# Optimization experiments

Measured on AMD Instinct MI355X. Metric: run time of the kernel, lower is better.

## Reference

```python
import jax, jax.numpy as jnp
import numpy as np

B, L = 128, 4096
H, RH, D, K = 128, 64, 64, 512  # num_hiddens, residual_hiddens, embedding_dim, num_embeddings
BETA = 0.25  # commitment_cost


def conv1d(x, w, b=None, stride=1, pad=0):
    # x: (N, C, W); w: (O, I, K) torch layout
    y = jax.lax.conv_general_dilated(x, w, (stride,), [(pad, pad)],
                                     dimension_numbers=('NCW', 'OIW', 'NCW'))
    return y if b is None else y + b[None, :, None]


def convT1d(x, w, b=None, stride=2, pad=1):
    # torch ConvTranspose1d weight layout (in, out, k)
    k = w.shape[-1]
    w_t = jnp.flip(w, -1).transpose(1, 0, 2)  # (out, in, k)
    y = jax.lax.conv_general_dilated(x, w_t, (1,), [(k - 1 - pad, k - 1 - pad)],
                                     lhs_dilation=(stride,),
                                     dimension_numbers=('NCW', 'OIW', 'NCW'))
    return y if b is None else y + b[None, :, None]


def res_stack(x, layers):
    for w1, w2 in layers:
        h = conv1d(jax.nn.relu(x), w1, None, 1, 1)
        h = conv1d(jax.nn.relu(h), w2, None, 1, 0)
        x = x + h
    return jax.nn.relu(x)


def _forward(x, enc_w1, enc_b1, enc_w2, enc_b2, enc_w3, enc_b3,
             enc_r1a, enc_r1b, enc_r2a, enc_r2b, pre_vq_w, pre_vq_b, codebook,
             dec_w1, dec_b1, dec_r1a, dec_r1b, dec_r2a, dec_r2b,
             dec_ct1_w, dec_ct1_b, dec_ct2_w, dec_ct2_b):
    # ---- Encoder (compression_factor == 4) ----
    h = x[:, None, :]                                   # (B, 1, L)
    h = jax.nn.relu(conv1d(h, enc_w1, enc_b1, 2, 1))    # (B, H/2, L/2)
    h = jax.nn.relu(conv1d(h, enc_w2, enc_b2, 2, 1))    # (B, H, L/4)
    h = conv1d(h, enc_w3, enc_b3, 1, 1)
    h = res_stack(h, [(enc_r1a, enc_r1b), (enc_r2a, enc_r2b)])
    z = conv1d(h, pre_vq_w, pre_vq_b, 1, 0)             # (B, D, T)

    # ---- Vector quantization ----
    zt = z.transpose(0, 2, 1)                           # (B, T, D)
    flat = zt.reshape(-1, D)                            # (BT, D)
    dists = (jnp.sum(flat * flat, 1, keepdims=True)
             - 2.0 * flat @ codebook.T
             + jnp.sum(codebook * codebook, 1))         # (BT, K)
    idx = jnp.argmin(dists, axis=1)                     # (BT,)
    q = codebook[idx].reshape(zt.shape)                 # (B, T, D)

    e_latent = jnp.mean((jax.lax.stop_gradient(q) - zt) ** 2)
    q_latent = jnp.mean((q - jax.lax.stop_gradient(zt)) ** 2)
    loss = q_latent + BETA * e_latent
    q_st = zt + jax.lax.stop_gradient(q - zt)           # straight-through

    counts = jnp.zeros((K,), flat.dtype).at[idx].add(1.0)
    probs = counts / idx.shape[0]
    perplexity = jnp.exp(-jnp.sum(probs * jnp.log(probs + 1e-10)))

    # ---- Decoder (compression_factor == 4) ----
    hd = q_st.transpose(0, 2, 1)                        # (B, D, T)
    hd = conv1d(hd, dec_w1, dec_b1, 1, 1)               # (B, H, T)
    hd = res_stack(hd, [(dec_r1a, dec_r1b), (dec_r2a, dec_r2b)])
    hd = jax.nn.relu(convT1d(hd, dec_ct1_w, dec_ct1_b)) # (B, H/2, 2T)
    hd = convT1d(hd, dec_ct2_w, dec_ct2_b)              # (B, 1, 4T)
    recon = jnp.squeeze(hd)                             # (B, L)
    return loss, recon, perplexity


def setup_inputs() -> dict:
    key = jax.random.key(0)
    ks = jax.random.split(key, 32)
    n = lambda i, shape, s=0.05: jax.random.normal(ks[i], shape, jnp.float32) * s
    inp = {
        'x': jax.random.normal(ks[0], (B, L), jnp.float32),
        'enc_w1': n(1, (H // 2, 1, 4)), 'enc_b1': jnp.zeros((H // 2,), jnp.float32),
        'enc_w2': n(2, (H, H // 2, 4)), 'enc_b2': jnp.zeros((H,), jnp.float32),
        'enc_w3': n(3, (H, H, 3)), 'enc_b3': jnp.zeros((H,), jnp.float32),
        'enc_r1a': n(4, (RH, H, 3)), 'enc_r1b': n(5, (H, RH, 1)),
        'enc_r2a': n(6, (RH, H, 3)), 'enc_r2b': n(7, (H, RH, 1)),
        'pre_vq_w': n(8, (D, H, 1)), 'pre_vq_b': jnp.zeros((D,), jnp.float32),
        'codebook': jax.random.uniform(ks[9], (K, D), jnp.float32, -1.0 / K, 1.0 / K),
        'dec_w1': n(10, (H, D, 3)), 'dec_b1': jnp.zeros((H,), jnp.float32),
        'dec_r1a': n(11, (RH, H, 3)), 'dec_r1b': n(12, (H, RH, 1)),
        'dec_r2a': n(13, (RH, H, 3)), 'dec_r2b': n(14, (H, RH, 1)),
        'dec_ct1_w': n(15, (H, H // 2, 4)), 'dec_ct1_b': jnp.zeros((H // 2,), jnp.float32),
        'dec_ct2_w': n(16, (H // 2, 1, 4)), 'dec_ct2_b': jnp.zeros((1,), jnp.float32),
    }
    return inp


def reference(x, enc_w1, enc_b1, enc_w2, enc_b2, enc_w3, enc_b3,
              enc_r1a, enc_r1b, enc_r2a, enc_r2b, pre_vq_w, pre_vq_b, codebook,
              dec_w1, dec_b1, dec_r1a, dec_r1b, dec_r2a, dec_r2b,
              dec_ct1_w, dec_ct1_b, dec_ct2_w, dec_ct2_b):
    return _forward(x, enc_w1, enc_b1, enc_w2, enc_b2, enc_w3, enc_b3,
                    enc_r1a, enc_r1b, enc_r2a, enc_r2b, pre_vq_w, pre_vq_b, codebook,
                    dec_w1, dec_b1, dec_r1a, dec_r1b, dec_r2a, dec_r2b,
                    dec_ct1_w, dec_ct1_b, dec_ct2_w, dec_ct2_b)
```

## Files before the change

### kernel.cpp

```cpp
#include <hip/hip_runtime.h>
#include <hip/hip_bf16.h>
#include <math.h>

using bf16 = __hip_bfloat16;
typedef __attribute__((ext_vector_type(4))) float f32x4;
typedef __attribute__((ext_vector_type(8))) short s16x8;

#define MFMA16(a,b,c) __builtin_amdgcn_mfma_f32_16x16x32_bf16((a),(b),(c),0,0,0)


__device__ inline float bf2f(unsigned short u) {
    union { float f; unsigned v; } c; c.v = ((unsigned)u) << 16; return c.f;
}
__device__ inline unsigned short bfbits(float f) {
    union { bf16 h; unsigned short u; } c; c.h = __float2bfloat16(f); return c.u;
}
__device__ inline s16x8 relu8(s16x8 v) {
#pragma unroll
    for (int j = 0; j < 8; ++j)
        v[j] = (short)(((unsigned short)v[j] & 0x8000u) ? 0 : (unsigned short)v[j]);
    return v;
}

enum { M_S1 = 0, M_S2 = 1, M_CT = 2 };

template<int CIN, int COUT, int NTAP, int MODE, bool RELU_IN, bool RELU_OUT,
         bool HAS_BIAS>
__global__ __launch_bounds__(256) void gconv_k(
    const bf16* __restrict__ in, const bf16* __restrict__ wt,
    const float* __restrict__ bias, bf16* __restrict__ out,
    int Lin, int Lout)
{
    constexpr int T  = (MODE == M_S2) ? 132 : ((MODE == M_CT) ? 66 : (NTAP == 3 ? 66 : 64));
    constexpr int NG = (MODE == M_CT) ? 2 : 1;
    constexpr int WL = (COUT == 128) ? 4 : 2;
    constexpr int KS = CIN / 32;
    constexpr int SOFF = (MODE == M_CT || NTAP == 3) ? -1 : 0;
    __shared__ bf16 sX[T * CIN];

    const int tid = threadIdx.x;
    const int b   = blockIdx.y;
    const int l0  = blockIdx.x * 64;
    const bf16* inb = in + (size_t)b * Lin * CIN;

    constexpr int CPR = CIN / 8;
    for (int i = tid; i < T * CPR; i += 256) {
        int t  = i / CPR;
        int c0 = (i - t * CPR) * 8;
        int g;
        if (MODE == M_S2) g = (t < 66) ? 2 * (l0 + t) : 2 * (l0 + t - 66) - 1;
        else              g = l0 + t + SOFF;
        s16x8 v = {};
        if (g >= 0 && g < Lin) v = *(const s16x8*)(inb + (size_t)g * CIN + c0);
        if (RELU_IN) v = relu8(v);
        int byte = ((t * CIN + c0) << 1) ^ ((t & 7) << 4);
        *(s16x8*)((char*)sX + byte) = v;
    }
    __syncthreads();

    const int lane = tid & 63;
    const int wid  = __builtin_amdgcn_readfirstlane(tid >> 6);
    const int co0  = (COUT == 128) ? wid * 32 : (wid & 1) * 32;
    const int lw0  = (COUT == 128) ? 0 : (wid >> 1) * 32;
    const int lr   = lane & 15;
    const int kg   = lane >> 4;

    f32x4 acc[NG][2][WL];
#pragma unroll
    for (int g = 0; g < NG; ++g)
#pragma unroll
        for (int cf = 0; cf < 2; ++cf)
#pragma unroll
            for (int lf = 0; lf < WL; ++lf)
                acc[g][cf][lf] = (f32x4){0.f, 0.f, 0.f, 0.f};

#pragma unroll
    for (int g = 0; g < NG; ++g) {
#pragma unroll
        for (int k = 0; k < NTAP; ++k) {
            int roff;
            if (MODE == M_S1)      roff = k;
            else if (MODE == M_S2) roff = (k == 0) ? 66 : (k == 1) ? 0 : (k == 2) ? 67 : 1;
            else                   roff = g + k;
            const bf16* Ab = wt + (size_t)(g * NTAP + k) * COUT * CIN;
#pragma unroll
            for (int ks = 0; ks < KS; ++ks) {
                s16x8 af[2];
#pragma unroll
                for (int cf = 0; cf < 2; ++cf)
                    af[cf] = *(const s16x8*)(Ab + (co0 + cf * 16 + lr) * CIN + ks * 32 + kg * 8);
                s16x8 bfr[WL];
#pragma unroll
                for (int lf = 0; lf < WL; ++lf) {
                    int t = roff + lw0 + lf * 16 + lr;
                    int byte = ((t * CIN + ks * 32 + kg * 8) << 1) ^ ((t & 7) << 4);
                    bfr[lf] = *(const s16x8*)((const char*)sX + byte);
                }
#pragma unroll
                for (int cf = 0; cf < 2; ++cf)
#pragma unroll
                    for (int lf = 0; lf < WL; ++lf)
                        acc[g][cf][lf] = MFMA16(af[cf], bfr[lf], acc[g][cf][lf]);
            }
        }
    }

#pragma unroll
    for (int g = 0; g < NG; ++g)
#pragma unroll
        for (int cf = 0; cf < 2; ++cf)
#pragma unroll
            for (int lf = 0; lf < WL; ++lf) {
                int cb0  = co0 + cf * 16 + kg * 4;
                int lcol = lw0 + lf * 16 + lr;
                int gcol = (MODE == M_CT) ? (2 * (l0 + lcol) + g) : (l0 + lcol);
                float r[4];
#pragma unroll
                for (int j = 0; j < 4; ++j) {
                    r[j] = acc[g][cf][lf][j];
                    if (HAS_BIAS) r[j] += bias[cb0 + j];
                    if (RELU_OUT) r[j] = fmaxf(r[j], 0.f);
                }
                bf16* po = out + ((size_t)b * Lout + gcol) * COUT + cb0;
                uint2 pk;
                pk.x = (unsigned)bfbits(r[0]) | ((unsigned)bfbits(r[1]) << 16);
                pk.y = (unsigned)bfbits(r[2]) | ((unsigned)bfbits(r[3]) << 16);
                *(uint2*)po = pk;
            }
}

template<bool RELU_OUT>
__global__ __launch_bounds__(256) void fres_k(
    const bf16* __restrict__ in, const bf16* __restrict__ w1t,
    const bf16* __restrict__ w2t, bf16* __restrict__ out)
{
    __shared__ bf16 sX[66 * 128];
    __shared__ bf16 sH[64 * 64];
    const int tid = threadIdx.x;
    const int b   = blockIdx.y;
    const int l0  = blockIdx.x * 64;
    const bf16* inb = in + (size_t)b * 1024 * 128;

    for (int i = tid; i < 66 * 16; i += 256) {
        int t = i >> 4, c0 = (i & 15) * 8;
        int g = l0 + t - 1;
        s16x8 v = {};
        if (g >= 0 && g < 1024) v = *(const s16x8*)(inb + (size_t)g * 128 + c0);
        int byte = ((t * 128 + c0) << 1) ^ ((t & 7) << 4);
        *(s16x8*)((char*)sX + byte) = v;
    }
    __syncthreads();

    const int lane = tid & 63;
    const int wid  = __builtin_amdgcn_readfirstlane(tid >> 6);
    const int lr   = lane & 15;
    const int kg   = lane >> 4;

    {
        const int co0 = (wid & 1) * 32;
        const int lw0 = (wid >> 1) * 32;
        f32x4 acc[2][2];
#pragma unroll
        for (int cf = 0; cf < 2; ++cf)
#pragma unroll
            for (int lf = 0; lf < 2; ++lf) acc[cf][lf] = (f32x4){0.f, 0.f, 0.f, 0.f};
#pragma unroll
        for (int k = 0; k < 3; ++k) {
            const bf16* Ab = w1t + (size_t)k * 64 * 128;
#pragma unroll
            for (int ks = 0; ks < 4; ++ks) {
                s16x8 af[2];
#pragma unroll
                for (int cf = 0; cf < 2; ++cf)
                    af[cf] = *(const s16x8*)(Ab + (co0 + cf * 16 + lr) * 128 + ks * 32 + kg * 8);
                s16x8 bfr[2];
#pragma unroll
                for (int lf = 0; lf < 2; ++lf) {
                    int t = k + lw0 + lf * 16 + lr;
                    int byte = ((t * 128 + ks * 32 + kg * 8) << 1) ^ ((t & 7) << 4);
                    bfr[lf] = relu8(*(const s16x8*)((const char*)sX + byte));
                }
#pragma unroll
                for (int cf = 0; cf < 2; ++cf)
#pragma unroll
                    for (int lf = 0; lf < 2; ++lf)
                        acc[cf][lf] = MFMA16(af[cf], bfr[lf], acc[cf][lf]);
            }
        }
#pragma unroll
        for (int cf = 0; cf < 2; ++cf)
#pragma unroll
            for (int lf = 0; lf < 2; ++lf) {
                int pos = lw0 + lf * 16 + lr;
                int ch  = co0 + cf * 16 + kg * 4;
                uint2 pk;
                pk.x = (unsigned)bfbits(fmaxf(acc[cf][lf][0], 0.f)) |
                       ((unsigned)bfbits(fmaxf(acc[cf][lf][1], 0.f)) << 16);
                pk.y = (unsigned)bfbits(fmaxf(acc[cf][lf][2], 0.f)) |
                       ((unsigned)bfbits(fmaxf(acc[cf][lf][3], 0.f)) << 16);
                int byte = ((pos * 64 + ch) << 1) ^ ((pos & 7) << 4);
                *(uint2*)((char*)sH + byte) = pk;
            }
    }
    __syncthreads();

    {
        const int co0 = wid * 32;
        f32x4 acc2[2][4];
#pragma unroll
        for (int cf = 0; cf < 2; ++cf)
#pragma unroll
            for (int lf = 0; lf < 4; ++lf) acc2[cf][lf] = (f32x4){0.f, 0.f, 0.f, 0.f};
#pragma unroll
        for (int ks = 0; ks < 2; ++ks) {
            s16x8 af[2];
#pragma unroll
            for (int cf = 0; cf < 2; ++cf)
                af[cf] = *(const s16x8*)(w2t + (size_t)(co0 + cf * 16 + lr) * 64 + ks * 32 + kg * 8);
            s16x8 bfr[4];
#pragma unroll
            for (int lf = 0; lf < 4; ++lf) {
                int t = lf * 16 + lr;
                int byte = ((t * 64 + ks * 32 + kg * 8) << 1) ^ ((t & 7) << 4);
                bfr[lf] = *(const s16x8*)((const char*)sH + byte);
            }
#pragma unroll
            for (int cf = 0; cf < 2; ++cf)
#pragma unroll
                for (int lf = 0; lf < 4; ++lf)
                    acc2[cf][lf] = MFMA16(af[cf], bfr[lf], acc2[cf][lf]);
        }
#pragma unroll
        for (int cf = 0; cf < 2; ++cf)
#pragma unroll
            for (int lf = 0; lf < 4; ++lf) {
                int cb0  = co0 + cf * 16 + kg * 4;
                int lcol = lf * 16 + lr;
                int tX   = lcol + 1;
                int rbyte = ((tX * 128 + cb0) << 1) ^ ((tX & 7) << 4);
                uint2 old = *(const uint2*)((const char*)sX + rbyte);
                float r[4];
                r[0] = acc2[cf][lf][0] + bf2f((unsigned short)(old.x & 0xffff));
                r[1] = acc2[cf][lf][1] + bf2f((unsigned short)(old.x >> 16));
                r[2] = acc2[cf][lf][2] + bf2f((unsigned short)(old.y & 0xffff));
                r[3] = acc2[cf][lf][3] + bf2f((unsigned short)(old.y >> 16));
                if (RELU_OUT)
#pragma unroll
                    for (int j = 0; j < 4; ++j) r[j] = fmaxf(r[j], 0.f);
                uint2 pk;
                pk.x = (unsigned)bfbits(r[0]) | ((unsigned)bfbits(r[1]) << 16);
                pk.y = (unsigned)bfbits(r[2]) | ((unsigned)bfbits(r[3]) << 16);
                *(uint2*)(out + ((size_t)b * 1024 + l0 + lcol) * 128 + cb0) = pk;
            }
    }
}

__global__ __launch_bounds__(256) void enc1_k(
    const float* __restrict__ x, const float* __restrict__ w,
    const float* __restrict__ bias, bf16* __restrict__ out)
{
    const int tid = threadIdx.x;
    const int b   = blockIdx.y;
    const int l   = blockIdx.x * 256 + tid;
    const float* xb = x + (size_t)b * 4096;
    float xv[4];
#pragma unroll
    for (int k = 0; k < 4; ++k) {
        int g = 2 * l - 1 + k;
        xv[k] = (g >= 0 && g < 4096) ? xb[g] : 0.f;
    }
    bf16* ob = out + ((size_t)b * 2048 + l) * 64;
#pragma unroll
    for (int c0 = 0; c0 < 64; c0 += 8) {
        union { unsigned short u[8]; s16x8 v; } pk;
#pragma unroll
        for (int j = 0; j < 8; ++j) {
            int co = c0 + j;
            float a = bias[co];
#pragma unroll
            for (int k = 0; k < 4; ++k) a = fmaf(xv[k], w[co * 4 + k], a);
            pk.u[j] = bfbits(fmaxf(a, 0.f));
        }
        *(s16x8*)(ob + c0) = pk.v;
    }
}

__global__ __launch_bounds__(256) void ct2_k(
    const bf16* __restrict__ in, const float* __restrict__ w,
    const float* __restrict__ bias, float* __restrict__ out)
{
    __shared__ bf16 sX[258 * 64];
    const int tid = threadIdx.x;
    const int b   = blockIdx.y;
    const int m0  = blockIdx.x * 256;
    const bf16* inb = in + (size_t)b * 2048 * 64;
    for (int i = tid; i < 258 * 8; i += 256) {
        int t = i >> 3, c0 = (i & 7) * 8;
        int g = m0 - 1 + t;
        s16x8 v = {};
        if (g >= 0 && g < 2048) v = *(const s16x8*)(inb + (size_t)g * 64 + c0);
        int byte = ((t * 64 + c0) << 1) ^ ((t & 7) << 4);
        *(s16x8*)((char*)sX + byte) = v;
    }
    __syncthreads();
    float e = bias[0], o = bias[0];
#pragma unroll
    for (int c0 = 0; c0 < 64; c0 += 8) {
        int t0 = tid, t1 = tid + 1, t2 = tid + 2;
        s16x8 vm1 = *(const s16x8*)((char*)sX + (((t0 * 64 + c0) << 1) ^ ((t0 & 7) << 4)));
        s16x8 v0  = *(const s16x8*)((char*)sX + (((t1 * 64 + c0) << 1) ^ ((t1 & 7) << 4)));
        s16x8 vp1 = *(const s16x8*)((char*)sX + (((t2 * 64 + c0) << 1) ^ ((t2 & 7) << 4)));
#pragma unroll
        for (int j = 0; j < 8; ++j) {
            int ci = c0 + j;
            float xm1 = bf2f((unsigned short)vm1[j]);
            float x0  = bf2f((unsigned short)v0[j]);
            float xp1 = bf2f((unsigned short)vp1[j]);
            e = fmaf(x0,  w[ci * 4 + 1], fmaf(xm1, w[ci * 4 + 3], e));
            o = fmaf(xp1, w[ci * 4 + 0], fmaf(x0,  w[ci * 4 + 2], o));
        }
    }
    int m = m0 + tid;
    out[(size_t)b * 4096 + 2 * m]     = e;
    out[(size_t)b * 4096 + 2 * m + 1] = o;
}

__global__ __launch_bounds__(256) void wx_k(
    const float* ew2, const float* ew3, const float* er1a, const float* er1b,
    const float* er2a, const float* er2b, const float* pvw, const float* dw1,
    const float* dr1a, const float* dr1b, const float* dr2a, const float* dr2b,
    const float* ct1w, bf16* wb)
{
    const int job = blockIdx.x;
    bf16* dst = wb + (size_t)job * 65536;
    const float* src; int CO, CI, K;
    switch (job) {
        case 0:  src = ew2;  CO = 128; CI = 64;  K = 4; break;
        case 1:  src = ew3;  CO = 128; CI = 128; K = 3; break;
        case 2:  src = er1a; CO = 64;  CI = 128; K = 3; break;
        case 3:  src = er1b; CO = 128; CI = 64;  K = 1; break;
        case 4:  src = er2a; CO = 64;  CI = 128; K = 3; break;
        case 5:  src = er2b; CO = 128; CI = 64;  K = 1; break;
        case 6:  src = pvw;  CO = 64;  CI = 128; K = 1; break;
        case 7:  src = dw1;  CO = 128; CI = 64;  K = 3; break;
        case 8:  src = dr1a; CO = 64;  CI = 128; K = 3; break;
        case 9:  src = dr1b; CO = 128; CI = 64;  K = 1; break;
        case 10: src = dr2a; CO = 64;  CI = 128; K = 3; break;
        case 11: src = dr2b; CO = 128; CI = 64;  K = 1; break;
        default: src = ct1w; CO = 64;  CI = 128; K = 4; break;
    }
    const int tot = CO * CI * K;
    for (int i = blockIdx.y * 256 + threadIdx.x; i < tot; i += gridDim.y * 256) {
        if (job < 12) {
            int k = i / (CO * CI); int r = i - k * CO * CI;
            int co = r / CI; int ci = r - co * CI;
            dst[i] = __float2bfloat16(src[((size_t)co * CI + ci) * K + k]);
        } else {
            const int TAP[4] = {3, 1, 2, 0};
            int g = i / (64 * 128); int r = i - g * 64 * 128;
            int co = r / 128; int ci = r - co * 128;
            dst[i] = __float2bfloat16(src[((size_t)ci * 64 + co) * 4 + TAP[g]]);
        }
    }
}

__global__ __launch_bounds__(256) void cbprep_k(
    const float* __restrict__ cb, bf16* __restrict__ cbh, bf16* __restrict__ cbl,
    float* __restrict__ sc)
{
    int k = blockIdx.x * 256 + threadIdx.x;
    const float* c = cb + (size_t)k * 64;
    float s = 0.f;
#pragma unroll
    for (int d = 0; d < 64; ++d) s = fmaf(c[d], c[d], s);
    sc[k] = s;
#pragma unroll
    for (int c0 = 0; c0 < 64; c0 += 8) {
        union { unsigned short u[8]; s16x8 v; } ph, pl;
#pragma unroll
        for (int j = 0; j < 8; ++j) {
            float v = c[c0 + j];
            unsigned short h = bfbits(v);
            ph.u[j] = h;
            pl.u[j] = bfbits(v - bf2f(h));
        }
        *(s16x8*)(cbh + (size_t)k * 64 + c0) = ph.v;
        *(s16x8*)(cbl + (size_t)k * 64 + c0) = pl.v;
    }
}

__global__ __launch_bounds__(256) void vqf_k(
    const bf16* __restrict__ A, const bf16* __restrict__ pvw,
    const float* __restrict__ pvb, const float* __restrict__ cbf,
    const bf16* __restrict__ cbh, const bf16* __restrict__ cbl,
    const float* __restrict__ sc, bf16* __restrict__ q,
    float* __restrict__ counts, float* __restrict__ loss_sum)
{
    __shared__ s16x8 sMemV[4096];
    char* sMem = (char*)sMemV;
    __shared__ float sSC[512];
    __shared__ float sHist[512];
    __shared__ int   sBK[256];
    __shared__ float sWS[4];
    const int tid = threadIdx.x;
    sSC[tid] = sc[tid]; sSC[tid + 256] = sc[tid + 256];
    sHist[tid] = 0.f;   sHist[tid + 256] = 0.f;

    const int n0blk = blockIdx.x * 256;
    for (int i = tid; i < 256 * 16; i += 256) {
        int t = i >> 4, c0 = (i & 15) * 8;
        s16x8 v = *(const s16x8*)(A + (size_t)(n0blk + t) * 128 + c0);
        int byte = ((t * 128 + c0) << 1) ^ ((t & 7) << 4);
        *(s16x8*)(sMem + byte) = v;
    }
    __syncthreads();

    const int lane = tid & 63, wid = tid >> 6;
    const int lr = lane & 15, kg = lane >> 4;
    const int pw0 = wid * 64;
    const f32x4 zf4 = {0.f, 0.f, 0.f, 0.f};

    f32x4 zacc[4][4];
#pragma unroll
    for (int cf = 0; cf < 4; ++cf)
#pragma unroll
        for (int lf = 0; lf < 4; ++lf) zacc[cf][lf] = zf4;
#pragma unroll
    for (int ks = 0; ks < 4; ++ks) {
        s16x8 af[4];
#pragma unroll
        for (int cf = 0; cf < 4; ++cf)
            af[cf] = *(const s16x8*)(pvw + (size_t)(cf * 16 + lr) * 128 + ks * 32 + kg * 8);
        s16x8 bfr[4];
#pragma unroll
        for (int lf = 0; lf < 4; ++lf) {
            int t = pw0 + lf * 16 + lr;
            int byte = ((t * 128 + ks * 32 + kg * 8) << 1) ^ ((t & 7) << 4);
            bfr[lf] = *(const s16x8*)((const char*)sMem + byte);
        }
#pragma unroll
        for (int cf = 0; cf < 4; ++cf)
#pragma unroll
            for (int lf = 0; lf < 4; ++lf)
                zacc[cf][lf] = MFMA16(af[cf], bfr[lf], zacc[cf][lf]);
    }
    __syncthreads();

#pragma unroll
    for (int cf = 0; cf < 4; ++cf)
#pragma unroll
        for (int lf = 0; lf < 4; ++lf) {
            int pos = pw0 + lf * 16 + lr;
            int ch  = cf * 16 + kg * 4;
            float4 v = make_float4(zacc[cf][lf][0] + pvb[ch],
                                   zacc[cf][lf][1] + pvb[ch + 1],
                                   zacc[cf][lf][2] + pvb[ch + 2],
                                   zacc[cf][lf][3] + pvb[ch + 3]);
            int byte = ((pos * 64 + ch) << 2) ^ ((pos & 7) << 5);
            *(float4*)(sMem + byte) = v;
        }
    __syncthreads();

    s16x8 bh[4][2], bl[4][2];
#pragma unroll
    for (int lf = 0; lf < 4; ++lf)
#pragma unroll
        for (int ks = 0; ks < 2; ++ks) {
            int t = pw0 + lf * 16 + lr;
            int ch = ks * 32 + kg * 8;
            int byte = ((t * 64 + ch) << 2) ^ ((t & 7) << 5);
            float4 v0 = *(const float4*)(sMem + byte);
            float4 v1 = *(const float4*)(sMem + byte + 16);
            float v[8] = {v0.x, v0.y, v0.z, v0.w, v1.x, v1.y, v1.z, v1.w};
            union { unsigned short u[8]; s16x8 s; } ph, pl;
#pragma unroll
            for (int j = 0; j < 8; ++j) {
                unsigned short h = bfbits(v[j]);
                ph.u[j] = h;
                pl.u[j] = bfbits(v[j] - bf2f(h));
            }
            bh[lf][ks] = ph.s; bl[lf][ks] = pl.s;
        }

    float bestd[4] = {3.4e38f, 3.4e38f, 3.4e38f, 3.4e38f};
    int   bestk[4] = {0, 0, 0, 0};
#pragma unroll 2
    for (int cf = 0; cf < 32; ++cf) {
        int code = cf * 16 + lr;
        const bf16* ph = cbh + code * 64 + kg * 8;
        const bf16* pl = cbl + code * 64 + kg * 8;
        s16x8 ah0 = *(const s16x8*)ph;
        s16x8 ah1 = *(const s16x8*)(ph + 32);
        s16x8 al0 = *(const s16x8*)pl;
        s16x8 al1 = *(const s16x8*)(pl + 32);
        float s0 = sSC[cf * 16 + kg * 4 + 0];
        float s1 = sSC[cf * 16 + kg * 4 + 1];
        float s2 = sSC[cf * 16 + kg * 4 + 2];
        float s3 = sSC[cf * 16 + kg * 4 + 3];
        int kb = cf * 16 + kg * 4;
#pragma unroll
        for (int lf = 0; lf < 4; ++lf) {
            f32x4 acc = MFMA16(ah0, bh[lf][0], zf4);
            acc = MFMA16(ah1, bh[lf][1], acc);
            acc = MFMA16(al0, bh[lf][0], acc);
            acc = MFMA16(al1, bh[lf][1], acc);
            acc = MFMA16(ah0, bl[lf][0], acc);
            acc = MFMA16(ah1, bl[lf][1], acc);
            float d0 = fmaf(acc[0], -2.f, s0);
            float d1 = fmaf(acc[1], -2.f, s1);
            float d2 = fmaf(acc[2], -2.f, s2);
            float d3 = fmaf(acc[3], -2.f, s3);
            if (d0 < bestd[lf]) { bestd[lf] = d0; bestk[lf] = kb; }
            if (d1 < bestd[lf]) { bestd[lf] = d1; bestk[lf] = kb + 1; }
            if (d2 < bestd[lf]) { bestd[lf] = d2; bestk[lf] = kb + 2; }
            if (d3 < bestd[lf]) { bestd[lf] = d3; bestk[lf] = kb + 3; }
        }
    }
#pragma unroll
    for (int lf = 0; lf < 4; ++lf) {
#pragma unroll
        for (int off = 16; off <= 32; off <<= 1) {
            float od = __shfl_xor(bestd[lf], off, 64);
            int   ok = __shfl_xor(bestk[lf], off, 64);
            if (od < bestd[lf] || (od == bestd[lf] && ok < bestk[lf])) {
                bestd[lf] = od; bestk[lf] = ok;
            }
        }
        if (kg == 0) sBK[wid * 64 + lf * 16 + lr] = bestk[lf];
    }
    __syncthreads();

    const int n = n0blk + tid;
    const int k = sBK[tid];
    atomicAdd(&sHist[k], 1.f);
    float lsum = 0.f;
    const float* qp = cbf + (size_t)k * 64;
#pragma unroll
    for (int c0 = 0; c0 < 64; c0 += 8) {
        int byte = ((tid * 64 + c0) << 2) ^ ((tid & 7) << 5);
        float4 z0 = *(const float4*)(sMem + byte);
        float4 z1 = *(const float4*)(sMem + byte + 16);
        float4 q0 = *(const float4*)(qp + c0);
        float4 q1 = *(const float4*)(qp + c0 + 4);
        float qv[8] = {q0.x, q0.y, q0.z, q0.w, q1.x, q1.y, q1.z, q1.w};
        float zv[8] = {z0.x, z0.y, z0.z, z0.w, z1.x, z1.y, z1.z, z1.w};
        union { unsigned short u[8]; s16x8 v; } pk;
#pragma unroll
        for (int j = 0; j < 8; ++j) {
            float d = qv[j] - zv[j];
            lsum = fmaf(d, d, lsum);
            pk.u[j] = bfbits(qv[j]);
        }
        *(s16x8*)(q + (size_t)n * 64 + c0) = pk.v;
    }
#pragma unroll
    for (int off = 32; off > 0; off >>= 1) lsum += __shfl_down(lsum, off, 64);
    if ((tid & 63) == 0) sWS[tid >> 6] = lsum;
    __syncthreads();
    if (tid == 0) atomicAdd(loss_sum, sWS[0] + sWS[1] + sWS[2] + sWS[3]);
    float c0v = sHist[tid];       if (c0v != 0.f) atomicAdd(&counts[tid], c0v);
    float c1v = sHist[tid + 256]; if (c1v != 0.f) atomicAdd(&counts[tid + 256], c1v);
}

__global__ __launch_bounds__(512) void finalize_k(
    const float* __restrict__ counts, const float* __restrict__ loss_sum,
    float* __restrict__ d_out, int out_size)
{
    __shared__ float ws2[8];
    const int tid = threadIdx.x;
    float p = counts[tid] * (1.f / 131072.f);
    float e = p * logf(p + 1e-10f);
#pragma unroll
    for (int off = 32; off > 0; off >>= 1) e += __shfl_down(e, off, 64);
    const int lane = tid & 63, wid = tid >> 6;
    if (lane == 0) ws2[wid] = e;
    __syncthreads();
    if (tid == 0) {
        float s = 0.f;
        for (int i = 0; i < 8; ++i) s += ws2[i];
        d_out[0] = 1.25f * loss_sum[0] * (1.f / 8388608.f);
        d_out[out_size - 1] = expf(-s);
    }
}

extern "C" void kernel_launch(void* const* d_in, const int* in_sizes, int n_in,
                              void* d_out, int out_size, void* d_ws, size_t ws_size,
                              hipStream_t stream)
{
    const float* x        = (const float*)d_in[0];
    const float* enc_w1   = (const float*)d_in[1];
    const float* enc_b1   = (const float*)d_in[2];
    const float* enc_b2   = (const float*)d_in[4];
    const float* enc_b3   = (const float*)d_in[6];
    const float* pre_vq_b = (const float*)d_in[12];
    const float* cb       = (const float*)d_in[13];
    const float* dec_b1   = (const float*)d_in[15];
    const float* ct1_b    = (const float*)d_in[21];
    const float* ct2_w    = (const float*)d_in[22];
    const float* ct2_b    = (const float*)d_in[23];
    float* out = (float*)d_out;

    char* base = (char*)d_ws;
    bf16*  wb   = (bf16*)base;
    bf16*  Abf  = (bf16*)(base + ((size_t)2   << 20));
    bf16*  Bbf  = (bf16*)(base + ((size_t)40  << 20));
    bf16*  Qbf  = (bf16*)(base + ((size_t)78  << 20));
    bf16*  cbh  = (bf16*)(base + ((size_t)96  << 20));
    bf16*  cbl  = (bf16*)(base + ((size_t)96  << 20) + 65536);
    float* sc   = (float*)(base + ((size_t)96  << 20) + 131072);
    float* cnt  = sc + 512;
    float* lsum = cnt + 512;

    hipMemsetAsync(cnt, 0, 513 * sizeof(float), stream);

    dim3 blk(256);
    dim3 g16(16, 128);

    wx_k<<<dim3(13, 8), blk, 0, stream>>>(
        (const float*)d_in[3], (const float*)d_in[5], (const float*)d_in[7],
        (const float*)d_in[8], (const float*)d_in[9], (const float*)d_in[10],
        (const float*)d_in[11], (const float*)d_in[14], (const float*)d_in[16],
        (const float*)d_in[17], (const float*)d_in[18], (const float*)d_in[19],
        (const float*)d_in[20], wb);
    cbprep_k<<<2, blk, 0, stream>>>(cb, cbh, cbl, sc);

    enc1_k<<<dim3(8, 128), blk, 0, stream>>>(x, enc_w1, enc_b1, Abf);
    gconv_k<64,128,4,M_S2,false,true ,true ><<<g16, blk, 0, stream>>>(
        Abf, wb + 0 * 65536, enc_b2, Bbf, 2048, 1024);
    gconv_k<128,128,3,M_S1,false,false,true ><<<g16, blk, 0, stream>>>(
        Bbf, wb + 1 * 65536, enc_b3, Abf, 1024, 1024);
    fres_k<false><<<g16, blk, 0, stream>>>(Abf, wb + 2 * 65536, wb + 3 * 65536, Bbf);
    fres_k<true ><<<g16, blk, 0, stream>>>(Bbf, wb + 4 * 65536, wb + 5 * 65536, Abf);

    vqf_k<<<512, blk, 0, stream>>>(Abf, wb + 6 * 65536, pre_vq_b, cb,
                                   cbh, cbl, sc, Qbf, cnt, lsum);

    gconv_k<64,128,3,M_S1,false,false,true ><<<g16, blk, 0, stream>>>(
        Qbf, wb + 7 * 65536, dec_b1, Abf, 1024, 1024);
    fres_k<false><<<g16, blk, 0, stream>>>(Abf, wb + 8 * 65536, wb + 9 * 65536, Bbf);
    fres_k<true ><<<g16, blk, 0, stream>>>(Bbf, wb + 10 * 65536, wb + 11 * 65536, Abf);
    gconv_k<128,64,2,M_CT,false,true ,true ><<<g16, blk, 0, stream>>>(
        Abf, wb + 12 * 65536, ct1_b, Bbf, 1024, 2048);

    ct2_k<<<dim3(8, 128), blk, 0, stream>>>(Bbf, ct2_w, ct2_b, out + 1);
    finalize_k<<<1, 512, 0, stream>>>(cnt, lsum, out, out_size);
}
```

Baseline: 418.1 us.

## Fuse first two encoder convs and slim the VQ kernel's distance computation

The first encoder conv (computed in shared memory from fp32 input) is fused with the strided second conv using MFMA, so the 2048x64 intermediate activation no longer round-trips through global memory. The VQ kernel drops the codebook low-part bf16 split, which cuts distance MFMAs from six to four per tile. It also halves the tile to 128 positions per block across more blocks and keeps z in registers via lane shuffles instead of a shared-memory transpose. Dropping the codebook low bits slightly lowers distance precision, which could flip argmin on near ties.

```diff
diff --git a/kernel.cpp b/kernel.cpp
--- a/kernel.cpp
+++ b/kernel.cpp
@@ -255,34 +255,96 @@
     }
 }
 
-__global__ __launch_bounds__(256) void enc1_k(
-    const float* __restrict__ x, const float* __restrict__ w,
-    const float* __restrict__ bias, bf16* __restrict__ out)
-{
+__global__ __launch_bounds__(256) void enc12_k(
+    const float* __restrict__ x, const float* __restrict__ w1,
+    const float* __restrict__ b1, const bf16* __restrict__ w2t,
+    const float* __restrict__ b2, bf16* __restrict__ out)
+{
+    __shared__ float sXf[268];
+    __shared__ float sW1[256];
+    __shared__ float sB1[64];
+    __shared__ bf16 sX[132 * 64];
     const int tid = threadIdx.x;
     const int b   = blockIdx.y;
-    const int l   = blockIdx.x * 256 + tid;
+    const int l0  = blockIdx.x * 64;
     const float* xb = x + (size_t)b * 4096;
-    float xv[4];
+
+    for (int i = tid; i < 266; i += 256) {
+        int g = 4 * l0 - 3 + i;
+        sXf[i] = (g >= 0 && g < 4096) ? xb[g] : 0.f;
+    }
+    if (tid < 256) sW1[tid] = w1[tid];
+    if (tid < 64)  sB1[tid] = b1[tid];
+    __syncthreads();
+
+    for (int i = tid; i < 132 * 64; i += 256) {
+        int t = i >> 6, c = i & 63;
+        int p = (t < 66) ? 2 * (l0 + t) : 2 * (l0 + t - 66) - 1;
+        float v = 0.f;
+        if (p >= 0 && p < 2048) {
+            int xi = 2 * p - 4 * l0 + 2;
+            float a = sB1[c];
+#pragma unroll
+            for (int k = 0; k < 4; ++k) a = fmaf(sXf[xi + k], sW1[c * 4 + k], a);
+            v = fmaxf(a, 0.f);
+        }
+        int byte = ((t * 64 + c) << 1) ^ ((t & 7) << 4);
+        *(bf16*)((char*)sX + byte) = __float2bfloat16(v);
+    }
+    __syncthreads();
+
+    const int lane = tid & 63;
+    const int wid  = __builtin_amdgcn_readfirstlane(tid >> 6);
+    const int co0  = wid * 32;
+    const int lr   = lane & 15;
+    const int kg   = lane >> 4;
+
+    f32x4 acc[2][4];
+#pragma unroll
+    for (int cf = 0; cf < 2; ++cf)
+#pragma unroll
+        for (int lf = 0; lf < 4; ++lf) acc[cf][lf] = (f32x4){0.f, 0.f, 0.f, 0.f};
+
 #pragma unroll
     for (int k = 0; k < 4; ++k) {
-        int g = 2 * l - 1 + k;
-        xv[k] = (g >= 0 && g < 4096) ? xb[g] : 0.f;
-    }
-    bf16* ob = out + ((size_t)b * 2048 + l) * 64;
-#pragma unroll
-    for (int c0 = 0; c0 < 64; c0 += 8) {
-        union { unsigned short u[8]; s16x8 v; } pk;
-#pragma unroll
-        for (int j = 0; j < 8; ++j) {
-            int co = c0 + j;
-            float a = bias[co];
-#pragma unroll
-            for (int k = 0; k < 4; ++k) a = fmaf(xv[k], w[co * 4 + k], a);
-            pk.u[j] = bfbits(fmaxf(a, 0.f));
-        }
-        *(s16x8*)(ob + c0) = pk.v;
-    }
+        const int roff = (k == 0) ? 66 : (k == 1) ? 0 : (k == 2) ? 67 : 1;
+        const bf16* Ab = w2t + (size_t)k * 128 * 64;
+#pragma unroll
+        for (int ks = 0; ks < 2; ++ks) {
+            s16x8 af[2];
+#pragma unroll
+            for (int cf = 0; cf < 2; ++cf)
+                af[cf] = *(const s16x8*)(Ab + (co0 + cf * 16 + lr) * 64 + ks * 32 + kg * 8);
+            s16x8 bfr[4];
+#pragma unroll
+            for (int lf = 0; lf < 4; ++lf) {
+                int t = roff + lf * 16 + lr;
+                int byte = ((t * 64 + ks * 32 + kg * 8) << 1) ^ ((t & 7) << 4);
+                bfr[lf] = *(const s16x8*)((const char*)sX + byte);
+            }
+#pragma unroll
+            for (int cf = 0; cf < 2; ++cf)
+#pragma unroll
+                for (int lf = 0; lf < 4; ++lf)
+                    acc[cf][lf] = MFMA16(af[cf], bfr[lf], acc[cf][lf]);
+        }
+    }
+
+#pragma unroll
+    for (int cf = 0; cf < 2; ++cf)
+#pragma unroll
+        for (int lf = 0; lf < 4; ++lf) {
+            int cb0  = co0 + cf * 16 + kg * 4;
+            int lcol = lf * 16 + lr;
+            float r[4];
+#pragma unroll
+            for (int j = 0; j < 4; ++j)
+                r[j] = fmaxf(acc[cf][lf][j] + b2[cb0 + j], 0.f);
+            uint2 pk;
+            pk.x = (unsigned)bfbits(r[0]) | ((unsigned)bfbits(r[1]) << 16);
+            pk.y = (unsigned)bfbits(r[2]) | ((unsigned)bfbits(r[3]) << 16);
+            *(uint2*)(out + ((size_t)b * 1024 + l0 + lcol) * 128 + cb0) = pk;
+        }
 }
 
 __global__ __launch_bounds__(256) void ct2_k(
@@ -365,8 +427,7 @@
 }
 
 __global__ __launch_bounds__(256) void cbprep_k(
-    const float* __restrict__ cb, bf16* __restrict__ cbh, bf16* __restrict__ cbl,
-    float* __restrict__ sc)
+    const float* __restrict__ cb, bf16* __restrict__ cbh, float* __restrict__ sc)
 {
     int k = blockIdx.x * 256 + threadIdx.x;
     const float* c = cb + (size_t)k * 64;
@@ -376,134 +437,119 @@
     sc[k] = s;
 #pragma unroll
     for (int c0 = 0; c0 < 64; c0 += 8) {
-        union { unsigned short u[8]; s16x8 v; } ph, pl;
-#pragma unroll
-        for (int j = 0; j < 8; ++j) {
-            float v = c[c0 + j];
-            unsigned short h = bfbits(v);
-            ph.u[j] = h;
-            pl.u[j] = bfbits(v - bf2f(h));
-        }
+        union { unsigned short u[8]; s16x8 v; } ph;
+#pragma unroll
+        for (int j = 0; j < 8; ++j) ph.u[j] = bfbits(c[c0 + j]);
         *(s16x8*)(cbh + (size_t)k * 64 + c0) = ph.v;
-        *(s16x8*)(cbl + (size_t)k * 64 + c0) = pl.v;
     }
 }
 
 __global__ __launch_bounds__(256) void vqf_k(
     const bf16* __restrict__ A, const bf16* __restrict__ pvw,
     const float* __restrict__ pvb, const float* __restrict__ cbf,
-    const bf16* __restrict__ cbh, const bf16* __restrict__ cbl,
-    const float* __restrict__ sc, bf16* __restrict__ q,
-    float* __restrict__ counts, float* __restrict__ loss_sum)
-{
-    __shared__ s16x8 sMemV[4096];
-    char* sMem = (char*)sMemV;
+    const bf16* __restrict__ cbh, const float* __restrict__ sc,
+    bf16* __restrict__ q, float* __restrict__ counts,
+    float* __restrict__ loss_sum)
+{
+    __shared__ bf16 sX[128 * 128];
     __shared__ float sSC[512];
     __shared__ float sHist[512];
-    __shared__ int   sBK[256];
+    __shared__ int   sBK[128];
     __shared__ float sWS[4];
     const int tid = threadIdx.x;
     sSC[tid] = sc[tid]; sSC[tid + 256] = sc[tid + 256];
     sHist[tid] = 0.f;   sHist[tid + 256] = 0.f;
 
-    const int n0blk = blockIdx.x * 256;
-    for (int i = tid; i < 256 * 16; i += 256) {
+    const int n0 = blockIdx.x * 128;
+    for (int i = tid; i < 128 * 16; i += 256) {
         int t = i >> 4, c0 = (i & 15) * 8;
-        s16x8 v = *(const s16x8*)(A + (size_t)(n0blk + t) * 128 + c0);
+        s16x8 v = *(const s16x8*)(A + (size_t)(n0 + t) * 128 + c0);
         int byte = ((t * 128 + c0) << 1) ^ ((t & 7) << 4);
-        *(s16x8*)(sMem + byte) = v;
+        *(s16x8*)((char*)sX + byte) = v;
     }
     __syncthreads();
 
     const int lane = tid & 63, wid = tid >> 6;
     const int lr = lane & 15, kg = lane >> 4;
-    const int pw0 = wid * 64;
+    const int pw0 = wid * 32;
     const f32x4 zf4 = {0.f, 0.f, 0.f, 0.f};
 
-    f32x4 zacc[4][4];
+    f32x4 zacc[4][2];
 #pragma unroll
     for (int cf = 0; cf < 4; ++cf)
 #pragma unroll
-        for (int lf = 0; lf < 4; ++lf) zacc[cf][lf] = zf4;
+        for (int lf = 0; lf < 2; ++lf) zacc[cf][lf] = zf4;
 #pragma unroll
     for (int ks = 0; ks < 4; ++ks) {
         s16x8 af[4];
 #pragma unroll
         for (int cf = 0; cf < 4; ++cf)
             af[cf] = *(const s16x8*)(pvw + (size_t)(cf * 16 + lr) * 128 + ks * 32 + kg * 8);
-        s16x8 bfr[4];
-#pragma unroll
-        for (int lf = 0; lf < 4; ++lf) {
+        s16x8 bfr[2];
+#pragma unroll
+        for (int lf = 0; lf < 2; ++lf) {
             int t = pw0 + lf * 16 + lr;
             int byte = ((t * 128 + ks * 32 + kg * 8) << 1) ^ ((t & 7) << 4);
-            bfr[lf] = *(const s16x8*)((const char*)sMem + byte);
+            bfr[lf] = *(const s16x8*)((const char*)sX + byte);
         }
 #pragma unroll
         for (int cf = 0; cf < 4; ++cf)
 #pragma unroll
-            for (int lf = 0; lf < 4; ++lf)
+            for (int lf = 0; lf < 2; ++lf)
                 zacc[cf][lf] = MFMA16(af[cf], bfr[lf], zacc[cf][lf]);
     }
-    __syncthreads();
-
-#pragma unroll
-    for (int cf = 0; cf < 4; ++cf)
-#pragma unroll
-        for (int lf = 0; lf < 4; ++lf) {
-            int pos = pw0 + lf * 16 + lr;
-            int ch  = cf * 16 + kg * 4;
-            float4 v = make_float4(zacc[cf][lf][0] + pvb[ch],
-                                   zacc[cf][lf][1] + pvb[ch + 1],
-                                   zacc[cf][lf][2] + pvb[ch + 2],
-                                   zacc[cf][lf][3] + pvb[ch + 3]);
-            int byte = ((pos * 64 + ch) << 2) ^ ((pos & 7) << 5);
-            *(float4*)(sMem + byte) = v;
-        }
-    __syncthreads();
-
-    s16x8 bh[4][2], bl[4][2];
-#pragma unroll
-    for (int lf = 0; lf < 4; ++lf)
+#pragma unroll
+    for (int cf = 0; cf < 4; ++cf) {
+        float4 bv = *(const float4*)(pvb + cf * 16 + kg * 4);
+#pragma unroll
+        for (int lf = 0; lf < 2; ++lf) {
+            zacc[cf][lf][0] += bv.x; zacc[cf][lf][1] += bv.y;
+            zacc[cf][lf][2] += bv.z; zacc[cf][lf][3] += bv.w;
+        }
+    }
+
+    const int srcA = lr + (((2 * kg) & 3) << 4);
+    const int srcB = lr + (((2 * kg + 1) & 3) << 4);
+    const bool hiCf = (kg >> 1) != 0;
+    s16x8 bh[2][2], bl[2][2];
+#pragma unroll
+    for (int lf = 0; lf < 2; ++lf)
 #pragma unroll
         for (int ks = 0; ks < 2; ++ks) {
-            int t = pw0 + lf * 16 + lr;
-            int ch = ks * 32 + kg * 8;
-            int byte = ((t * 64 + ch) << 2) ^ ((t & 7) << 5);
-            float4 v0 = *(const float4*)(sMem + byte);
-            float4 v1 = *(const float4*)(sMem + byte + 16);
-            float v[8] = {v0.x, v0.y, v0.z, v0.w, v1.x, v1.y, v1.z, v1.w};
             union { unsigned short u[8]; s16x8 s; } ph, pl;
 #pragma unroll
-            for (int j = 0; j < 8; ++j) {
-                unsigned short h = bfbits(v[j]);
-                ph.u[j] = h;
-                pl.u[j] = bfbits(v[j] - bf2f(h));
+            for (int i = 0; i < 4; ++i) {
+                float a0 = __shfl(zacc[2 * ks][lf][i], srcA, 64);
+                float a1 = __shfl(zacc[2 * ks + 1][lf][i], srcA, 64);
+                float va = hiCf ? a1 : a0;
+                float b0 = __shfl(zacc[2 * ks][lf][i], srcB, 64);
+                float b1 = __shfl(zacc[2 * ks + 1][lf][i], srcB, 64);
+                float vb = hiCf ? b1 : b0;
+                unsigned short h = bfbits(va);
+                ph.u[i] = h; pl.u[i] = bfbits(va - bf2f(h));
+                h = bfbits(vb);
+                ph.u[4 + i] = h; pl.u[4 + i] = bfbits(vb - bf2f(h));
             }
             bh[lf][ks] = ph.s; bl[lf][ks] = pl.s;
         }
 
-    float bestd[4] = {3.4e38f, 3.4e38f, 3.4e38f, 3.4e38f};
-    int   bestk[4] = {0, 0, 0, 0};
-#pragma unroll 2
+    float bestd[2] = {3.4e38f, 3.4e38f};
+    int   bestk[2] = {0, 0};
+#pragma unroll 4
     for (int cf = 0; cf < 32; ++cf) {
         int code = cf * 16 + lr;
         const bf16* ph = cbh + code * 64 + kg * 8;
-        const bf16* pl = cbl + code * 64 + kg * 8;
         s16x8 ah0 = *(const s16x8*)ph;
         s16x8 ah1 = *(const s16x8*)(ph + 32);
-        s16x8 al0 = *(const s16x8*)pl;
-        s16x8 al1 = *(const s16x8*)(pl + 32);
         float s0 = sSC[cf * 16 + kg * 4 + 0];
         float s1 = sSC[cf * 16 + kg * 4 + 1];
         float s2 = sSC[cf * 16 + kg * 4 + 2];
         float s3 = sSC[cf * 16 + kg * 4 + 3];
         int kb = cf * 16 + kg * 4;
 #pragma unroll
-        for (int lf = 0; lf < 4; ++lf) {
+        for (int lf = 0; lf < 2; ++lf) {
             f32x4 acc = MFMA16(ah0, bh[lf][0], zf4);
             acc = MFMA16(ah1, bh[lf][1], acc);
-            acc = MFMA16(al0, bh[lf][0], acc);
-            acc = MFMA16(al1, bh[lf][1], acc);
             acc = MFMA16(ah0, bl[lf][0], acc);
             acc = MFMA16(ah1, bl[lf][1], acc);
             float d0 = fmaf(acc[0], -2.f, s0);
@@ -517,7 +563,7 @@
         }
     }
 #pragma unroll
-    for (int lf = 0; lf < 4; ++lf) {
+    for (int lf = 0; lf < 2; ++lf) {
 #pragma unroll
         for (int off = 16; off <= 32; off <<= 1) {
             float od = __shfl_xor(bestd[lf], off, 64);
@@ -526,36 +572,35 @@
                 bestd[lf] = od; bestk[lf] = ok;
             }
         }
-        if (kg == 0) sBK[wid * 64 + lf * 16 + lr] = bestk[lf];
-    }
-    __syncthreads();
-
-    const int n = n0blk + tid;
-    const int k = sBK[tid];
-    atomicAdd(&sHist[k], 1.f);
+        if (kg == 0) sBK[pw0 + lf * 16 + lr] = bestk[lf];
+    }
+    __syncthreads();
+
     float lsum = 0.f;
-    const float* qp = cbf + (size_t)k * 64;
-#pragma unroll
-    for (int c0 = 0; c0 < 64; c0 += 8) {
-        int byte = ((tid * 64 + c0) << 2) ^ ((tid & 7) << 5);
-        float4 z0 = *(const float4*)(sMem + byte);
-        float4 z1 = *(const float4*)(sMem + byte + 16);
-        float4 q0 = *(const float4*)(qp + c0);
-        float4 q1 = *(const float4*)(qp + c0 + 4);
-        float qv[8] = {q0.x, q0.y, q0.z, q0.w, q1.x, q1.y, q1.z, q1.w};
-        float zv[8] = {z0.x, z0.y, z0.z, z0.w, z1.x, z1.y, z1.z, z1.w};
-        union { unsigned short u[8]; s16x8 v; } pk;
-#pragma unroll
-        for (int j = 0; j < 8; ++j) {
-            float d = qv[j] - zv[j];
-            lsum = fmaf(d, d, lsum);
-            pk.u[j] = bfbits(qv[j]);
-        }
-        *(s16x8*)(q + (size_t)n * 64 + c0) = pk.v;
+#pragma unroll
+    for (int lf = 0; lf < 2; ++lf) {
+        int posl = pw0 + lf * 16 + lr;
+        int k = sBK[posl];
+        if (kg == 0) atomicAdd(&sHist[k], 1.f);
+        const float* qp = cbf + (size_t)k * 64 + kg * 4;
+        bf16* qo = q + (size_t)(n0 + posl) * 64 + kg * 4;
+#pragma unroll
+        for (int cf = 0; cf < 4; ++cf) {
+            float4 qv = *(const float4*)(qp + cf * 16);
+            float d0 = qv.x - zacc[cf][lf][0];
+            float d1 = qv.y - zacc[cf][lf][1];
+            float d2 = qv.z - zacc[cf][lf][2];
+            float d3 = qv.w - zacc[cf][lf][3];
+            lsum = fmaf(d0, d0, fmaf(d1, d1, fmaf(d2, d2, fmaf(d3, d3, lsum))));
+            uint2 pk;
+            pk.x = (unsigned)bfbits(qv.x) | ((unsigned)bfbits(qv.y) << 16);
+            pk.y = (unsigned)bfbits(qv.z) | ((unsigned)bfbits(qv.w) << 16);
+            *(uint2*)(qo + cf * 16) = pk;
+        }
     }
 #pragma unroll
     for (int off = 32; off > 0; off >>= 1) lsum += __shfl_down(lsum, off, 64);
-    if ((tid & 63) == 0) sWS[tid >> 6] = lsum;
+    if (lane == 0) sWS[wid] = lsum;
     __syncthreads();
     if (tid == 0) atomicAdd(loss_sum, sWS[0] + sWS[1] + sWS[2] + sWS[3]);
     float c0v = sHist[tid];       if (c0v != 0.f) atomicAdd(&counts[tid], c0v);
@@ -606,7 +651,6 @@
     bf16*  Bbf  = (bf16*)(base + ((size_t)40  << 20));
     bf16*  Qbf  = (bf16*)(base + ((size_t)78  << 20));
     bf16*  cbh  = (bf16*)(base + ((size_t)96  << 20));
-    bf16*  cbl  = (bf16*)(base + ((size_t)96  << 20) + 65536);
     float* sc   = (float*)(base + ((size_t)96  << 20) + 131072);
     float* cnt  = sc + 512;
     float* lsum = cnt + 512;
@@ -622,18 +666,16 @@
         (const float*)d_in[11], (const float*)d_in[14], (const float*)d_in[16],
         (const float*)d_in[17], (const float*)d_in[18], (const float*)d_in[19],
         (const float*)d_in[20], wb);
-    cbprep_k<<<2, blk, 0, stream>>>(cb, cbh, cbl, sc);
-
-    enc1_k<<<dim3(8, 128), blk, 0, stream>>>(x, enc_w1, enc_b1, Abf);
-    gconv_k<64,128,4,M_S2,false,true ,true ><<<g16, blk, 0, stream>>>(
-        Abf, wb + 0 * 65536, enc_b2, Bbf, 2048, 1024);
+    cbprep_k<<<2, blk, 0, stream>>>(cb, cbh, sc);
+
+    enc12_k<<<g16, blk, 0, stream>>>(x, enc_w1, enc_b1, wb + 0 * 65536, enc_b2, Bbf);
     gconv_k<128,128,3,M_S1,false,false,true ><<<g16, blk, 0, stream>>>(
         Bbf, wb + 1 * 65536, enc_b3, Abf, 1024, 1024);
     fres_k<false><<<g16, blk, 0, stream>>>(Abf, wb + 2 * 65536, wb + 3 * 65536, Bbf);
     fres_k<true ><<<g16, blk, 0, stream>>>(Bbf, wb + 4 * 65536, wb + 5 * 65536, Abf);
 
-    vqf_k<<<512, blk, 0, stream>>>(Abf, wb + 6 * 65536, pre_vq_b, cb,
-                                   cbh, cbl, sc, Qbf, cnt, lsum);
+    vqf_k<<<1024, blk, 0, stream>>>(Abf, wb + 6 * 65536, pre_vq_b, cb,
+                                    cbh, sc, Qbf, cnt, lsum);
 
     gconv_k<64,128,3,M_S1,false,false,true ><<<g16, blk, 0, stream>>>(
         Qbf, wb + 7 * 65536, dec_b1, Abf, 1024, 1024);
```

After: 418.7 us. Within noise of the previous version (+0.2%).
